# Kernel optimization log

Measured on AMD Instinct MI355X. Metric: run time of the kernel, lower is better.

## Reference

```python
import jax, jax.numpy as jnp
import numpy as np

B, H, W, C, WS, SHIFT, NH = 64, 14, 14, 1024, 7, 3, 32
HD = C // NH
SCALE = HD ** -0.5

def _rel_index():
    coords = np.stack(np.meshgrid(np.arange(WS), np.arange(WS), indexing='ij'))  # [2,ws,ws]
    flat = coords.reshape(2, -1)
    rel = (flat[:, :, None] - flat[:, None, :]).transpose(1, 2, 0)  # [49,49,2]
    rel[:, :, 0] += WS - 1
    rel[:, :, 1] += WS - 1
    rel[:, :, 0] *= 2 * WS - 1
    return jnp.asarray(rel.sum(-1))  # [49,49] int

REL_IDX = _rel_index()

def _shift_mask():
    m = np.zeros((H, W), np.float32)
    cnt = 0
    for hs in (slice(0, -WS), slice(-WS, -SHIFT), slice(-SHIFT, None)):
        for ws_ in (slice(0, -WS), slice(-WS, -SHIFT), slice(-SHIFT, None)):
            m[hs, ws_] = cnt
            cnt += 1
    mw = m.reshape(H // WS, WS, W // WS, WS).transpose(0, 2, 1, 3).reshape(-1, WS * WS)
    diff = mw[:, None, :] - mw[:, :, None]
    return jnp.asarray(np.where(diff != 0, -100.0, 0.0).astype(np.float32))  # [nW,49,49]

ATTN_MASK = _shift_mask()

def layernorm(x, g, b, eps=1e-5):
    mu = x.mean(-1, keepdims=True)
    var = ((x - mu) ** 2).mean(-1, keepdims=True)
    return (x - mu) * jax.lax.rsqrt(var + eps) * g + b

def window_partition(x):  # [B,H,W,C] -> [B*nW, 49, C]
    x = x.reshape(B, H // WS, WS, W // WS, WS, C)
    return x.transpose(0, 1, 3, 2, 4, 5).reshape(-1, WS * WS, C)

def window_reverse(x):  # [B*nW, 49, C] -> [B,H,W,C]
    x = x.reshape(B, H // WS, W // WS, WS, WS, C)
    return x.transpose(0, 1, 3, 2, 4, 5).reshape(B, H, W, C)

def swin_block(x, p, shift):
    (ln1_g, ln1_b, qkv_w, qkv_b, rpb, proj_w, proj_b,
     ln2_g, ln2_b, fc1_w, fc1_b, fc2_w, fc2_b) = p
    h = layernorm(x, ln1_g, ln1_b).reshape(B, H, W, C)
    if shift:
        h = jnp.roll(h, (-SHIFT, -SHIFT), axis=(1, 2))
    hw = window_partition(h)                              # [Bn,49,C]
    qkv = hw @ qkv_w + qkv_b                              # [Bn,49,3C]
    q, k, v = qkv.reshape(-1, WS * WS, 3, NH, HD).transpose(2, 0, 3, 1, 4)  # each [Bn,NH,49,HD]
    attn = jnp.einsum('bhqd,bhkd->bhqk', q * SCALE, k)    # [Bn,NH,49,49]
    attn = attn + rpb[REL_IDX].transpose(2, 0, 1)[None]   # fused rel-pos bias
    if shift:
        nW = ATTN_MASK.shape[0]
        attn = attn.reshape(B, nW, NH, WS * WS, WS * WS) + ATTN_MASK[None, :, None]
        attn = attn.reshape(-1, NH, WS * WS, WS * WS)
    attn = jax.nn.softmax(attn, axis=-1)
    o = jnp.einsum('bhqk,bhkd->bhqd', attn, v).transpose(0, 2, 1, 3).reshape(-1, WS * WS, C)
    o = o @ proj_w + proj_b
    o = window_reverse(o)
    if shift:
        o = jnp.roll(o, (SHIFT, SHIFT), axis=(1, 2))
    x = x + o.reshape(B, H * W, C)
    h2 = layernorm(x, ln2_g, ln2_b)
    return x + jax.nn.gelu(h2 @ fc1_w + fc1_b, approximate=False) @ fc2_w + fc2_b

def setup_inputs() -> dict:
    key = jax.random.key(0)
    ks = iter(jax.random.split(key, 64))
    def rnd(shape, s=0.02):
        return jax.random.normal(next(ks), shape, jnp.float32) * s
    inp = {'x': jax.random.normal(next(ks), (B, H * W, C), jnp.float32)}
    for i in range(2):
        inp[f'b{i}_ln1_g'] = jnp.ones((C,), jnp.float32)
        inp[f'b{i}_ln1_b'] = jnp.zeros((C,), jnp.float32)
        inp[f'b{i}_qkv_w'] = rnd((C, 3 * C))
        inp[f'b{i}_qkv_b'] = jnp.zeros((3 * C,), jnp.float32)
        inp[f'b{i}_rpb'] = rnd(((2 * WS - 1) ** 2, NH))
        inp[f'b{i}_proj_w'] = rnd((C, C))
        inp[f'b{i}_proj_b'] = jnp.zeros((C,), jnp.float32)
        inp[f'b{i}_ln2_g'] = jnp.ones((C,), jnp.float32)
        inp[f'b{i}_ln2_b'] = jnp.zeros((C,), jnp.float32)
        inp[f'b{i}_fc1_w'] = rnd((C, 4 * C))
        inp[f'b{i}_fc1_b'] = jnp.zeros((4 * C,), jnp.float32)
        inp[f'b{i}_fc2_w'] = rnd((4 * C, C))
        inp[f'b{i}_fc2_b'] = jnp.zeros((C,), jnp.float32)
    inp['h_ln_g'] = jnp.ones((C,), jnp.float32)
    inp['h_ln_b'] = jnp.zeros((C,), jnp.float32)
    inp['h_w1'] = rnd((C, 512)); inp['h_b1'] = jnp.zeros((512,), jnp.float32)
    inp['h_w2'] = rnd((512, 128)); inp['h_b2'] = jnp.zeros((128,), jnp.float32)
    inp['h_w3'] = rnd((128, 2)); inp['h_b3'] = jnp.zeros((2,), jnp.float32)
    return inp

def reference(x,
              b0_ln1_g, b0_ln1_b, b0_qkv_w, b0_qkv_b, b0_rpb, b0_proj_w, b0_proj_b,
              b0_ln2_g, b0_ln2_b, b0_fc1_w, b0_fc1_b, b0_fc2_w, b0_fc2_b,
              b1_ln1_g, b1_ln1_b, b1_qkv_w, b1_qkv_b, b1_rpb, b1_proj_w, b1_proj_b,
              b1_ln2_g, b1_ln2_b, b1_fc1_w, b1_fc1_b, b1_fc2_w, b1_fc2_b,
              h_ln_g, h_ln_b, h_w1, h_b1, h_w2, h_b2, h_w3, h_b3):
    p0 = (b0_ln1_g, b0_ln1_b, b0_qkv_w, b0_qkv_b, b0_rpb, b0_proj_w, b0_proj_b,
          b0_ln2_g, b0_ln2_b, b0_fc1_w, b0_fc1_b, b0_fc2_w, b0_fc2_b)
    p1 = (b1_ln1_g, b1_ln1_b, b1_qkv_w, b1_qkv_b, b1_rpb, b1_proj_w, b1_proj_b,
          b1_ln2_g, b1_ln2_b, b1_fc1_w, b1_fc1_b, b1_fc2_w, b1_fc2_b)
    x = swin_block(x, p0, shift=False)
    x = swin_block(x, p1, shift=True)
    pooled = x.mean(axis=1)  # global avg pool -> [B, C]
    h = layernorm(pooled, h_ln_g, h_ln_b)
    h = jax.nn.gelu(h @ h_w1 + h_b1, approximate=False)  # dropout is identity (eval)
    h = jax.nn.gelu(h @ h_w2 + h_b2, approximate=False)
    return h @ h_w3 + h_b3  # [B, num_classes]
```

## Files before the change

kernel.cpp:

```cpp
#include <hip/hip_runtime.h>
#include <hip/hip_bf16.h>
#include <hip/hip_fp16.h>
#include <math.h>

#define BB 64
#define CC 1024
#define NH 32
#define NTOK (BB * 14 * 14)
#define SCALE 0.17677669529663687f

typedef __attribute__((ext_vector_type(8))) short short8;
typedef __attribute__((ext_vector_type(8))) unsigned short us8;
typedef __attribute__((ext_vector_type(4))) float f32x4;

__device__ __align__(16) float  g_X  [(size_t)NTOK * CC];
__device__ __align__(16) float  g_QKV[(size_t)NTOK * 3072];
__device__ __align__(16) unsigned short g_B[(size_t)NTOK * CC];
__device__ __align__(16) unsigned short g_C[(size_t)NTOK * 4096];
__device__ __align__(16) unsigned short g_Wq[(size_t)2*3072*1024];
__device__ __align__(16) unsigned short g_Wp[(size_t)2*1024*1024];
__device__ __align__(16) unsigned short g_W1[(size_t)2*4096*1024];
__device__ __align__(16) unsigned short g_W2[(size_t)2*1024*4096];
__device__ __align__(16) float g_H0[64 * CC];
__device__ __align__(16) float g_H1[64 * 512];
__device__ __align__(16) float g_H2[64 * 128];

__device__ __forceinline__ float gelu_f(float x) {
    return 0.5f * x * (1.0f + erff(x * 0.70710678118654752f));
}

__device__ __forceinline__ unsigned short f16_bits(float v) {
    _Float16 hh = (_Float16)v;
    return *(unsigned short*)&hh;
}

__device__ __forceinline__ int win_to_xrow(int r, int shifted) {
    int bn = r / 49, t = r - bn * 49;
    int b = bn >> 2, w = bn & 3;
    int wh = w >> 1, ww_ = w & 1;
    int th = t / 7, tw = t - th * 7;
    int gh = wh * 7 + th, gw = ww_ * 7 + tw;
    if (shifted) { gh = gh + 3; if (gh >= 14) gh -= 14; gw = gw + 3; if (gw >= 14) gw -= 14; }
    return b * 196 + gh * 14 + gw;
}

__device__ __forceinline__ void gload_lds16(const void* g, void* l) {
    __builtin_amdgcn_global_load_lds(
        (const __attribute__((address_space(1))) unsigned int*)g,
        (__attribute__((address_space(3))) unsigned int*)l, 16, 0, 0);
}

__global__ __launch_bounds__(256) void convw_kernel(const float* __restrict__ W,
    unsigned short* __restrict__ Wh, int K, int N)
{
    __shared__ float t[32][33];
    int n0 = blockIdx.x * 32, k0 = blockIdx.y * 32;
    int tx = threadIdx.x & 31, ty = threadIdx.x >> 5;
    #pragma unroll
    for (int i = 0; i < 4; ++i)
        t[ty + 8 * i][tx] = W[(size_t)(k0 + ty + 8 * i) * N + n0 + tx];
    __syncthreads();
    #pragma unroll
    for (int i = 0; i < 4; ++i) {
        int n = ty + 8 * i;
        Wh[(size_t)(n0 + n) * K + k0 + tx] = f16_bits(t[tx][n]);
    }
}

__global__ __launch_bounds__(256) void ln_kernel(const float* __restrict__ X,
    const float* __restrict__ g, const float* __restrict__ bta,
    unsigned short* __restrict__ outh, int shifted, int partition)
{
    int token = blockIdx.x * 4 + (threadIdx.x >> 6);
    int lane = threadIdx.x & 63;
    int xrow = partition ? win_to_xrow(token, shifted) : token;
    const float4* src = (const float4*)(X + (size_t)xrow * CC);
    float4 v[4];
    float s = 0.f;
    #pragma unroll
    for (int w = 0; w < 4; ++w) {
        v[w] = src[w * 64 + lane];
        s += v[w].x + v[w].y + v[w].z + v[w].w;
    }
    #pragma unroll
    for (int o = 32; o; o >>= 1) s += __shfl_xor(s, o);
    float mean = s * (1.0f / CC);
    float ss = 0.f;
    #pragma unroll
    for (int w = 0; w < 4; ++w) {
        float d0 = v[w].x - mean, d1 = v[w].y - mean, d2 = v[w].z - mean, d3 = v[w].w - mean;
        ss += d0 * d0 + d1 * d1 + d2 * d2 + d3 * d3;
    }
    #pragma unroll
    for (int o = 32; o; o >>= 1) ss += __shfl_xor(ss, o);
    float inv = 1.0f / sqrtf(ss * (1.0f / CC) + 1e-5f);
    #pragma unroll
    for (int w = 0; w < 4; ++w) {
        int c4 = w * 64 + lane;
        float4 gv = *(const float4*)(g + c4 * 4);
        float4 bv = *(const float4*)(bta + c4 * 4);
        ushort4 uo;
        uo.x = f16_bits((v[w].x - mean) * inv * gv.x + bv.x);
        uo.y = f16_bits((v[w].y - mean) * inv * gv.y + bv.y);
        uo.z = f16_bits((v[w].z - mean) * inv * gv.z + bv.z);
        uo.w = f16_bits((v[w].w - mean) * inv * gv.w + bv.w);
        *(ushort4*)(outh + (size_t)token * CC + c4 * 4) = uo;
    }
}

template<int EPI>
__global__ __launch_bounds__(256, 2) void gemm_mfma(
    const unsigned short* __restrict__ A, const unsigned short* __restrict__ W,
    const float* __restrict__ bias,
    float* __restrict__ outf, unsigned short* __restrict__ outh,
    int N, int K, int shifted, int NR, int GC)
{
    __shared__ unsigned short sm[16896];
    const int tid = threadIdx.x;
    const int wave = tid >> 6, lane = tid & 63;
    const int wr = wave >> 1, wc = wave & 1;
    const int nb = gridDim.x;
    const int wg = (blockIdx.x & 7) * (nb >> 3) + (blockIdx.x >> 3);
    const int gsz = GC * NR;
    const int grp = wg / gsz;
    const int rem = wg - grp * gsz;
    const int by = rem / GC;
    const int bx = grp * GC + (rem - by * GC);
    const int row0 = by * 128, col0 = bx * 128;
    const int rsel = lane & 15;

    f32x4 acc[4][4] = {};

    const int srow = tid >> 3, sslot = tid & 7;

    for (int k0 = 0; k0 < K; k0 += 64) {
        #pragma unroll
        for (int i = 0; i < 8; ++i) {
            const int t = i >> 2;
            const int sub = i & 3;
            const int row = sub * 32 + srow;
            const int c = sslot ^ (row & 7);
            const unsigned short* gp = (t == 0) ? A : W;
            const int rb = (t == 0) ? row0 : col0;
            gload_lds16(gp + (size_t)(rb + row) * K + k0 + c * 8,
                        &sm[t * 8192 + sub * 2048 + tid * 8]);
        }
        __syncthreads();

        #pragma unroll
        for (int kk = 0; kk < 2; ++kk) {
            const int kc8 = kk * 4 + (lane >> 4);
            short8 fa[4], fw[4];
            #pragma unroll
            for (int m = 0; m < 4; ++m) {
                int ra = wr * 64 + m * 16 + rsel;
                fa[m] = *(const short8*)&sm[ra * 64 + ((kc8 ^ (ra & 7)) * 8)];
                int rw = wc * 64 + m * 16 + rsel;
                fw[m] = *(const short8*)&sm[8192 + rw * 64 + ((kc8 ^ (rw & 7)) * 8)];
            }
            #pragma unroll
            for (int m = 0; m < 4; ++m)
                #pragma unroll
                for (int n = 0; n < 4; ++n)
                    acc[m][n] = __builtin_amdgcn_mfma_f32_16x16x32_f16(fa[m], fw[n], acc[m][n], 0, 0, 0);
        }
        __syncthreads();
    }

    const int jrow = lane >> 4;
    if (EPI == 1) {
        #pragma unroll
        for (int n = 0; n < 4; ++n) {
            int cl = wc * 64 + n * 16 + rsel;
            float bv = bias[col0 + cl];
            #pragma unroll
            for (int m = 0; m < 4; ++m)
                #pragma unroll
                for (int j = 0; j < 4; ++j) {
                    int rl = wr * 64 + m * 16 + jrow * 4 + j;
                    sm[rl * 132 + cl] = f16_bits(gelu_f(acc[m][n][j] + bv));
                }
        }
        __syncthreads();
        const int r = tid >> 1, cb = (tid & 1) * 64;
        unsigned short* dst = outh + (size_t)(row0 + r) * N + col0 + cb;
        const unsigned short* src = &sm[r * 132 + cb];
        #pragma unroll
        for (int i = 0; i < 8; ++i)
            *(us8*)(dst + i * 8) = *(const us8*)(src + i * 8);
    } else {
        #pragma unroll
        for (int n = 0; n < 4; ++n) {
            int c = col0 + wc * 64 + n * 16 + rsel;
            float bv = bias[c];
            #pragma unroll
            for (int m = 0; m < 4; ++m) {
                #pragma unroll
                for (int j = 0; j < 4; ++j) {
                    int r = row0 + wr * 64 + m * 16 + jrow * 4 + j;
                    float v = acc[m][n][j] + bv;
                    if (EPI == 0) {
                        outf[(size_t)r * N + c] = v;
                    } else if (EPI == 2) {
                        outf[(size_t)win_to_xrow(r, shifted) * CC + c] += v;
                    } else {
                        outf[(size_t)r * CC + c] += v;
                    }
                }
            }
        }
    }
}

__global__ __launch_bounds__(64) void attn_kernel(const float* __restrict__ qkv,
    unsigned short* __restrict__ oh, const float* __restrict__ rpb, int shifted)
{
    int bh = blockIdx.x;
    int bn = bh >> 5, h = bh & 31;
    __shared__ float qs[49][32], ks[49][32], vs[49][32];
    __shared__ float ss[49][50];
    int lane = threadIdx.x;
    for (int idx = lane; idx < 49 * 32; idx += 64) {
        int t = idx >> 5, d = idx & 31;
        const float* p = qkv + (size_t)(bn * 49 + t) * 3072 + h * 32 + d;
        qs[t][d] = p[0];
        ks[t][d] = p[1024];
        vs[t][d] = p[2048];
    }
    __syncthreads();
    if (lane < 49) {
        int i = lane;
        int ih = i / 7, iw = i - ih * 7;
        int w = bn & 3, wh = w >> 1, ww_ = w & 1;
        int gh = wh * 7 + ih, gw = ww_ * 7 + iw;
        int li = (gh < 7 ? 0 : (gh < 11 ? 1 : 2)) * 3 + (gw < 7 ? 0 : (gw < 11 ? 1 : 2));
        float qreg[32];
        #pragma unroll
        for (int d = 0; d < 32; ++d) qreg[d] = qs[i][d] * SCALE;
        float mx = -1e30f;
        for (int j = 0; j < 49; ++j) {
            int jh = j / 7, jw = j - jh * 7;
            float dot = 0.f;
            #pragma unroll
            for (int d = 0; d < 32; ++d) dot = fmaf(qreg[d], ks[j][d], dot);
            int ridx = (ih - jh + 6) * 13 + (iw - jw + 6);
            float val = dot + rpb[ridx * 32 + h];
            if (shifted) {
                int gjh = wh * 7 + jh, gjw = ww_ * 7 + jw;
                int lj = (gjh < 7 ? 0 : (gjh < 11 ? 1 : 2)) * 3 +
                         (gjw < 7 ? 0 : (gjw < 11 ? 1 : 2));
                if (li != lj) val -= 100.0f;
            }
            ss[i][j] = val;
            mx = fmaxf(mx, val);
        }
        float denom = 0.f;
        for (int j = 0; j < 49; ++j) {
            float e = expf(ss[i][j] - mx);
            ss[i][j] = e;
            denom += e;
        }
        float rd = 1.0f / denom;
        size_t obase = (size_t)(bn * 49 + i) * CC + h * 32;
        #pragma unroll 4
        for (int d = 0; d < 32; ++d) {
            float acc = 0.f;
            for (int j = 0; j < 49; ++j) acc = fmaf(ss[i][j], vs[j][d], acc);
            oh[obase + d] = f16_bits(acc * rd);
        }
    }
}

__global__ __launch_bounds__(256) void pool_ln_kernel(const float* __restrict__ X,
    const float* __restrict__ g, const float* __restrict__ bta, float* __restrict__ out)
{
    int b = blockIdx.x, tid = threadIdx.x;
    int lane = tid & 63, wid = tid >> 6;
    const float* base = X + (size_t)b * 196 * CC + tid * 4;
    float a0 = 0, a1 = 0, a2 = 0, a3 = 0;
    for (int t = 0; t < 196; ++t) {
        float4 v = *(const float4*)(base + (size_t)t * CC);
        a0 += v.x; a1 += v.y; a2 += v.z; a3 += v.w;
    }
    const float inv196 = 1.0f / 196.0f;
    float p0 = a0 * inv196, p1 = a1 * inv196, p2 = a2 * inv196, p3 = a3 * inv196;
    float s = p0 + p1 + p2 + p3;
    #pragma unroll
    for (int o = 32; o; o >>= 1) s += __shfl_xor(s, o);
    __shared__ float sred[4], ssred[4];
    if (lane == 0) sred[wid] = s;
    __syncthreads();
    float mean = (sred[0] + sred[1] + sred[2] + sred[3]) * (1.0f / CC);
    float d0 = p0 - mean, d1 = p1 - mean, d2 = p2 - mean, d3 = p3 - mean;
    float ss = d0 * d0 + d1 * d1 + d2 * d2 + d3 * d3;
    #pragma unroll
    for (int o = 32; o; o >>= 1) ss += __shfl_xor(ss, o);
    if (lane == 0) ssred[wid] = ss;
    __syncthreads();
    float var = (ssred[0] + ssred[1] + ssred[2] + ssred[3]) * (1.0f / CC);
    float inv = 1.0f / sqrtf(var + 1e-5f);
    float4 gv = *(const float4*)(g + tid * 4);
    float4 bv = *(const float4*)(bta + tid * 4);
    float4 o4;
    o4.x = d0 * inv * gv.x + bv.x;
    o4.y = d1 * inv * gv.y + bv.y;
    o4.z = d2 * inv * gv.z + bv.z;
    o4.w = d3 * inv * gv.w + bv.w;
    *(float4*)(out + (size_t)b * CC + tid * 4) = o4;
}

__global__ __launch_bounds__(256) void head_rowgemm(const float* __restrict__ A,
    const float* __restrict__ W, const float* __restrict__ bias,
    float* __restrict__ out, int K, int N, int act)
{
    __shared__ float As[1024];
    int r = blockIdx.x, tid = threadIdx.x;
    for (int k = tid; k < K; k += 256) As[k] = A[(size_t)r * K + k];
    __syncthreads();
    for (int c = tid; c < N; c += 256) {
        float s0 = 0.f, s1 = 0.f;
        for (int k = 0; k < K; k += 2) {
            s0 = fmaf(As[k],     W[(size_t)k * N + c],       s0);
            s1 = fmaf(As[k + 1], W[(size_t)(k + 1) * N + c], s1);
        }
        float s = s0 + s1 + bias[c];
        out[(size_t)r * N + c] = act ? gelu_f(s) : s;
    }
}

extern "C" void kernel_launch(void* const* d_in, const int* in_sizes, int n_in,
                              void* d_out, int out_size, void* d_ws, size_t ws_size,
                              hipStream_t stream) {
    const float* x = (const float*)d_in[0];
    auto P = [&](int i) { return (const float*)d_in[i]; };

    float *X, *QKV, *H0, *H1, *H2;
    unsigned short *B, *C, *Wq, *Wp, *W1, *W2;
    { void* p;
      hipGetSymbolAddress(&p, HIP_SYMBOL(g_X));   X   = (float*)p;
      hipGetSymbolAddress(&p, HIP_SYMBOL(g_QKV)); QKV = (float*)p;
      hipGetSymbolAddress(&p, HIP_SYMBOL(g_B));   B   = (unsigned short*)p;
      hipGetSymbolAddress(&p, HIP_SYMBOL(g_C));   C   = (unsigned short*)p;
      hipGetSymbolAddress(&p, HIP_SYMBOL(g_Wq));  Wq  = (unsigned short*)p;
      hipGetSymbolAddress(&p, HIP_SYMBOL(g_Wp));  Wp  = (unsigned short*)p;
      hipGetSymbolAddress(&p, HIP_SYMBOL(g_W1));  W1  = (unsigned short*)p;
      hipGetSymbolAddress(&p, HIP_SYMBOL(g_W2));  W2  = (unsigned short*)p;
      hipGetSymbolAddress(&p, HIP_SYMBOL(g_H0));  H0 = (float*)p;
      hipGetSymbolAddress(&p, HIP_SYMBOL(g_H1));  H1 = (float*)p;
      hipGetSymbolAddress(&p, HIP_SYMBOL(g_H2));  H2 = (float*)p;
    }

    hipMemcpyAsync(X, x, (size_t)NTOK * CC * sizeof(float),
                   hipMemcpyDeviceToDevice, stream);

    for (int blk = 0; blk < 2; ++blk) {
        int base = 1 + blk * 13;
        convw_kernel<<<dim3(3072/32, 1024/32), 256, 0, stream>>>(
            P(base + 2), Wq + (size_t)blk*3072*1024, 1024, 3072);
        convw_kernel<<<dim3(1024/32, 1024/32), 256, 0, stream>>>(
            P(base + 5), Wp + (size_t)blk*1024*1024, 1024, 1024);
        convw_kernel<<<dim3(4096/32, 1024/32), 256, 0, stream>>>(
            P(base + 9), W1 + (size_t)blk*4096*1024, 1024, 4096);
        convw_kernel<<<dim3(1024/32, 4096/32), 256, 0, stream>>>(
            P(base + 11), W2 + (size_t)blk*1024*4096, 4096, 1024);
    }

    for (int blk = 0; blk < 2; ++blk) {
        int base = 1 + blk * 13;
        const float *ln1g = P(base + 0), *ln1b = P(base + 1);
        const float *qkvb = P(base + 3);
        const float *rpb  = P(base + 4);
        const float *projb = P(base + 6);
        const float *ln2g = P(base + 7), *ln2b = P(base + 8);
        const float *fc1b = P(base + 10);
        const float *fc2b = P(base + 12);
        int shifted = blk;
        const unsigned short* wq = Wq + (size_t)blk*3072*1024;
        const unsigned short* wp = Wp + (size_t)blk*1024*1024;
        const unsigned short* w1 = W1 + (size_t)blk*4096*1024;
        const unsigned short* w2 = W2 + (size_t)blk*1024*4096;

        ln_kernel<<<NTOK / 4, 256, 0, stream>>>(X, ln1g, ln1b, B, shifted, 1);
        gemm_mfma<0><<<2352, 256, 0, stream>>>(
            B, wq, qkvb, QKV, nullptr, 3072, 1024, 0, 98, 8);
        attn_kernel<<<256 * NH, 64, 0, stream>>>(QKV, B, rpb, shifted);
        gemm_mfma<2><<<784, 256, 0, stream>>>(
            B, wp, projb, X, nullptr, 1024, 1024, shifted, 98, 8);
        ln_kernel<<<NTOK / 4, 256, 0, stream>>>(X, ln2g, ln2b, B, 0, 0);
        gemm_mfma<1><<<3136, 256, 0, stream>>>(
            B, w1, fc1b, nullptr, C, 4096, 1024, 0, 98, 8);
        gemm_mfma<3><<<784, 256, 0, stream>>>(
            C, w2, fc2b, X, nullptr, 1024, 4096, 0, 98, 2);
    }

    pool_ln_kernel<<<64, 256, 0, stream>>>(X, P(27), P(28), H0);
    head_rowgemm<<<64, 256, 0, stream>>>(H0, P(29), P(30), H1, 1024, 512, 1);
    head_rowgemm<<<64, 256, 0, stream>>>(H1, P(31), P(32), H2, 512, 128, 1);
    head_rowgemm<<<64, 256, 0, stream>>>(H2, P(33), P(34), (float*)d_out, 128, 2, 0);
}
```

Baseline: 1.502 ms.

## Restructure window attention to four heads per block with register-held scores

The attention kernel now runs four heads per 256-thread block, one wave per head, instead of one 64-thread block per head. Q is read straight from global memory into registers with float4 loads rather than staged through shared memory. The score row is kept in a fully unrolled 49-element register array instead of a shared-memory matrix. Separately, the GEMM shared buffer is trimmed for every epilogue except the FC1 one. The aim is fewer, fuller blocks and less LDS traffic, at the cost of much higher register pressure that may spill or lower occupancy.

```diff
diff --git a/kernel.cpp b/kernel.cpp
--- a/kernel.cpp
+++ b/kernel.cpp
@@ -115,7 +115,7 @@
     float* __restrict__ outf, unsigned short* __restrict__ outh,
     int N, int K, int shifted, int NR, int GC)
 {
-    __shared__ unsigned short sm[16896];
+    __shared__ unsigned short sm[EPI == 1 ? 16896 : 16384];
     const int tid = threadIdx.x;
     const int wave = tid >> 6, lane = tid & 63;
     const int wr = wave >> 1, wc = wave & 1;
@@ -212,61 +212,78 @@
     }
 }
 
-__global__ __launch_bounds__(64) void attn_kernel(const float* __restrict__ qkv,
+__global__ __launch_bounds__(256) void attn_kernel(const float* __restrict__ qkv,
     unsigned short* __restrict__ oh, const float* __restrict__ rpb, int shifted)
 {
-    int bh = blockIdx.x;
-    int bn = bh >> 5, h = bh & 31;
-    __shared__ float qs[49][32], ks[49][32], vs[49][32];
-    __shared__ float ss[49][50];
-    int lane = threadIdx.x;
+    int blk = blockIdx.x;
+    int bn = blk >> 3;
+    int hg = blk & 7;
+    int wv = threadIdx.x >> 6;
+    int lane = threadIdx.x & 63;
+    int h = hg * 4 + wv;
+
+    __shared__ float ks[4][49][32], vs[4][49][32];
+
     for (int idx = lane; idx < 49 * 32; idx += 64) {
         int t = idx >> 5, d = idx & 31;
         const float* p = qkv + (size_t)(bn * 49 + t) * 3072 + h * 32 + d;
-        qs[t][d] = p[0];
-        ks[t][d] = p[1024];
-        vs[t][d] = p[2048];
+        ks[wv][t][d] = p[1024];
+        vs[wv][t][d] = p[2048];
     }
     __syncthreads();
+
     if (lane < 49) {
-        int i = lane;
-        int ih = i / 7, iw = i - ih * 7;
-        int w = bn & 3, wh = w >> 1, ww_ = w & 1;
-        int gh = wh * 7 + ih, gw = ww_ * 7 + iw;
-        int li = (gh < 7 ? 0 : (gh < 11 ? 1 : 2)) * 3 + (gw < 7 ? 0 : (gw < 11 ? 1 : 2));
+        const int i = lane;
+        const int ih = i / 7, iw = i - ih * 7;
+        const int w = bn & 3, wh = w >> 1, ww_ = w & 1;
+        const int gh = wh * 7 + ih, gw = ww_ * 7 + iw;
+        const int li = (gh < 7 ? 0 : (gh < 11 ? 1 : 2)) * 3 + (gw < 7 ? 0 : (gw < 11 ? 1 : 2));
+
         float qreg[32];
-        #pragma unroll
-        for (int d = 0; d < 32; ++d) qreg[d] = qs[i][d] * SCALE;
+        const float* qp = qkv + (size_t)(bn * 49 + i) * 3072 + h * 32;
+        #pragma unroll
+        for (int d4 = 0; d4 < 8; ++d4) {
+            float4 qv = *(const float4*)(qp + d4 * 4);
+            qreg[d4 * 4 + 0] = qv.x * SCALE;
+            qreg[d4 * 4 + 1] = qv.y * SCALE;
+            qreg[d4 * 4 + 2] = qv.z * SCALE;
+            qreg[d4 * 4 + 3] = qv.w * SCALE;
+        }
+
+        float p[49];
         float mx = -1e30f;
+        #pragma unroll
         for (int j = 0; j < 49; ++j) {
-            int jh = j / 7, jw = j - jh * 7;
+            const int jh = j / 7, jw = j - jh * 7;
             float dot = 0.f;
             #pragma unroll
-            for (int d = 0; d < 32; ++d) dot = fmaf(qreg[d], ks[j][d], dot);
-            int ridx = (ih - jh + 6) * 13 + (iw - jw + 6);
+            for (int d = 0; d < 32; ++d) dot = fmaf(qreg[d], ks[wv][j][d], dot);
+            const int ridx = (ih - jh + 6) * 13 + (iw - jw + 6);
             float val = dot + rpb[ridx * 32 + h];
             if (shifted) {
-                int gjh = wh * 7 + jh, gjw = ww_ * 7 + jw;
-                int lj = (gjh < 7 ? 0 : (gjh < 11 ? 1 : 2)) * 3 +
-                         (gjw < 7 ? 0 : (gjw < 11 ? 1 : 2));
+                const int gjh = wh * 7 + jh, gjw = ww_ * 7 + jw;
+                const int lj = (gjh < 7 ? 0 : (gjh < 11 ? 1 : 2)) * 3 +
+                               (gjw < 7 ? 0 : (gjw < 11 ? 1 : 2));
                 if (li != lj) val -= 100.0f;
             }
-            ss[i][j] = val;
+            p[j] = val;
             mx = fmaxf(mx, val);
         }
         float denom = 0.f;
+        #pragma unroll
         for (int j = 0; j < 49; ++j) {
-            float e = expf(ss[i][j] - mx);
-            ss[i][j] = e;
-            denom += e;
-        }
-        float rd = 1.0f / denom;
-        size_t obase = (size_t)(bn * 49 + i) * CC + h * 32;
+            p[j] = expf(p[j] - mx);
+            denom += p[j];
+        }
+        const float rd = 1.0f / denom;
+
+        unsigned short* orow = oh + (size_t)(bn * 49 + i) * CC + h * 32;
         #pragma unroll 4
         for (int d = 0; d < 32; ++d) {
             float acc = 0.f;
-            for (int j = 0; j < 49; ++j) acc = fmaf(ss[i][j], vs[j][d], acc);
-            oh[obase + d] = f16_bits(acc * rd);
+            #pragma unroll
+            for (int j = 0; j < 49; ++j) acc = fmaf(p[j], vs[wv][j][d], acc);
+            orow[d] = f16_bits(acc * rd);
         }
     }
 }
@@ -383,7 +400,7 @@
         ln_kernel<<<NTOK / 4, 256, 0, stream>>>(X, ln1g, ln1b, B, shifted, 1);
         gemm_mfma<0><<<2352, 256, 0, stream>>>(
             B, wq, qkvb, QKV, nullptr, 3072, 1024, 0, 98, 8);
-        attn_kernel<<<256 * NH, 64, 0, stream>>>(QKV, B, rpb, shifted);
+        attn_kernel<<<256 * 8, 256, 0, stream>>>(QKV, B, rpb, shifted);
         gemm_mfma<2><<<784, 256, 0, stream>>>(
             B, wp, projb, X, nullptr, 1024, 1024, shifted, 98, 8);
         ln_kernel<<<NTOK / 4, 256, 0, stream>>>(X, ln2g, ln2b, B, 0, 0);
```

Result: slower. 1.579 ms (+5.1%).
